# Performance work log

Hardware: AMD Instinct MI355X
Metric: run time of the kernel (lower is better)

## Reference

```python
import jax, jax.numpy as jnp
import numpy as np

NUM_CENTROID = 64
HIDDEN = 768
MAX_SEQ = 128
D = MAX_SEQ * HIDDEN  # 98304 flattened feature dim
NUM_ITERS = 10        # fixed Lloyd iterations (original loops to tol; fixed for jit)


def _cdist(x, c):
    x2 = jnp.sum(x * x, axis=-1, keepdims=True)          # [N,1]
    c2 = jnp.sum(c * c, axis=-1)                          # [K]
    d2 = x2 + c2[None, :] - 2.0 * (x @ c.T)               # [N,K]
    return jnp.sqrt(jnp.maximum(d2, 0.0))


def setup_inputs() -> dict:
    key = jax.random.key(0)
    k1, k2 = jax.random.split(key)
    x = jax.random.normal(k1, (1024, MAX_SEQ, HIDDEN), dtype=jnp.float32)
    # centroid table initialized as Normal(mean=0.07, std=0.39) per the module
    centroid = 0.07 + 0.39 * jax.random.normal(k2, (NUM_CENTROID, D), dtype=jnp.float32)
    return {"x": x, "centroid": centroid}


def reference(x, centroid):
    X = x.reshape(-1, D)                                  # [N, D]
    N = X.shape[0]
    # 'resuming' branch: snap each centroid to its nearest sample
    dis0 = _cdist(X, centroid)                            # [N, K]
    choice_points = jnp.argmin(dis0, axis=0)              # [K]
    state = X[choice_points]                              # [K, D]
    ones = jnp.ones((N,), dtype=X.dtype)

    def step(state, _):
        dis = _cdist(X, state)                            # [N, K]
        choice = jnp.argmin(dis, axis=1)                  # [N]
        sums = jax.ops.segment_sum(X, choice, num_segments=NUM_CENTROID)   # [K, D]
        counts = jax.ops.segment_sum(ones, choice, num_segments=NUM_CENTROID)  # [K]
        nonempty = counts[:, None] > 0
        new_state = jnp.where(nonempty, sums / jnp.maximum(counts[:, None], 1.0), state)
        return new_state, choice

    state, choices = jax.lax.scan(step, state, None, length=NUM_ITERS)
    # returns (new centroids, final cluster assignments) like the module
    return state, choices[-1]
```

## Files before the change

### kernel.cpp

```cpp
#include <hip/hip_runtime.h>
#include <cstddef>
#include <cstdint>


#define N_PTS  1024
#define K_C    64
#define D_DIM  98304
#define ITERS  10
#define SPLITD 64
#define BM     64
#define DC     64
#define LDSP   72
#define NCHK   96
#define CCHK   12
#define NGRP   16
#define SHPG   12
#define SHW    512
#define NCHT   192
#define NPAIR  36
#define GT     128
#define GDC    32

typedef __attribute__((ext_vector_type(8))) short bf16x8;
typedef __attribute__((ext_vector_type(8))) unsigned short ushort8;
typedef __attribute__((ext_vector_type(4))) float f32x4;

__device__ __forceinline__ unsigned short f2bf(float x) {
    unsigned u = __float_as_uint(x);
    u = (u + 0x7FFFu + ((u >> 16) & 1u)) >> 16;
    return (unsigned short)u;
}
__device__ __forceinline__ float bf2f(unsigned short b) {
    return __uint_as_float((unsigned)b << 16);
}
__device__ __forceinline__ void cvt2(float x, unsigned short& h, unsigned short& l) {
    h = f2bf(x);
    l = f2bf(x - bf2f(h));
}

__device__ __forceinline__ void gload_lds16(const unsigned short* g, char* l) {
    __builtin_amdgcn_global_load_lds(
        (const __attribute__((address_space(1))) unsigned int*)g,
        (__attribute__((address_space(3))) unsigned int*)l, 16, 0, 0);
}

__device__ __forceinline__ float block_sum256(float s) {
    #pragma unroll
    for (int o = 32; o; o >>= 1) s += __shfl_down(s, o);
    __shared__ float red[4];
    int lane = threadIdx.x & 63, w = threadIdx.x >> 6;
    if (lane == 0) red[w] = s;
    __syncthreads();
    return red[0] + red[1] + red[2] + red[3];
}

__global__ __launch_bounds__(256) void convert_kernel(const float* __restrict__ A,
                                                      unsigned short* __restrict__ Ph,
                                                      unsigned short* __restrict__ Pl,
                                                      float* __restrict__ sq_part) {
    const int n = blockIdx.x, j = blockIdx.y;
    const size_t base = (size_t)n * D_DIM + (size_t)j * 8192;
    const int t = threadIdx.x;
    float ss = 0.f;
    #pragma unroll
    for (int i = 0; i < 4; ++i) {
        size_t e = base + (size_t)i * 2048 + t * 8;
        float4 a = *reinterpret_cast<const float4*>(A + e);
        float4 b = *reinterpret_cast<const float4*>(A + e + 4);
        ss += a.x*a.x + a.y*a.y + a.z*a.z + a.w*a.w;
        ss += b.x*b.x + b.y*b.y + b.z*b.z + b.w*b.w;
        ushort4 h0, l0, h1, l1;
        cvt2(a.x, h0.x, l0.x); cvt2(a.y, h0.y, l0.y);
        cvt2(a.z, h0.z, l0.z); cvt2(a.w, h0.w, l0.w);
        cvt2(b.x, h1.x, l1.x); cvt2(b.y, h1.y, l1.y);
        cvt2(b.z, h1.z, l1.z); cvt2(b.w, h1.w, l1.w);
        *reinterpret_cast<ushort4*>(Ph + e)     = h0;
        *reinterpret_cast<ushort4*>(Ph + e + 4) = h1;
        *reinterpret_cast<ushort4*>(Pl + e)     = l0;
        *reinterpret_cast<ushort4*>(Pl + e + 4) = l1;
    }
    ss = block_sum256(ss);
    if (t == 0) sq_part[n * CCHK + j] = ss;
}

__global__ __launch_bounds__(256) void reduce_sq_kernel(const float* __restrict__ sq_part,
                                                        float* __restrict__ out, int rows) {
    int n = blockIdx.x * 256 + threadIdx.x;
    if (n >= rows) return;
    float s = 0.f;
    #pragma unroll
    for (int j = 0; j < CCHK; ++j) s += sq_part[n * CCHK + j];
    out[n] = s;
}

__global__ __launch_bounds__(256) void mfma_dot_kernel(const unsigned short* __restrict__ Xh,
                                                       const unsigned short* __restrict__ Xl,
                                                       const unsigned short* __restrict__ Sh,
                                                       const unsigned short* __restrict__ Sl,
                                                       float* __restrict__ partial) {
    __shared__ alignas(16) short Bh[K_C][LDSP];
    __shared__ alignas(16) short Bl[K_C][LDSP];

    const int seg = blockIdx.x, nblk = blockIdx.y;
    const int t = threadIdx.x;
    const int wid = t >> 6, lane = t & 63;
    const int d_begin = seg * (D_DIM / SPLITD);
    const int NCH = (D_DIM / SPLITD) / DC;

    const int arow = nblk * BM + wid * 16 + (lane & 15);
    const int ko = (lane >> 4) * 8;
    const unsigned short* xh = Xh + (size_t)arow * D_DIM;
    const unsigned short* xl = Xl + (size_t)arow * D_DIM;

    const int sr = t >> 2, sc = (t & 3) * 16;
    const unsigned short* shp = Sh + (size_t)sr * D_DIM;
    const unsigned short* slp = Sl + (size_t)sr * D_DIM;

    ushort8 s0, s1, s2, s3;
    bf16x8 aEh0, aEh1, aEl0, aEl1;
    bf16x8 aOh0, aOh1, aOl0, aOl1;

    auto loadB = [&](int d0) {
        s0 = *reinterpret_cast<const ushort8*>(shp + d0 + sc);
        s1 = *reinterpret_cast<const ushort8*>(shp + d0 + sc + 8);
        s2 = *reinterpret_cast<const ushort8*>(slp + d0 + sc);
        s3 = *reinterpret_cast<const ushort8*>(slp + d0 + sc + 8);
    };
    auto storeB = [&]() {
        *reinterpret_cast<ushort8*>(&Bh[sr][sc])     = s0;
        *reinterpret_cast<ushort8*>(&Bh[sr][sc + 8]) = s1;
        *reinterpret_cast<ushort8*>(&Bl[sr][sc])     = s2;
        *reinterpret_cast<ushort8*>(&Bl[sr][sc + 8]) = s3;
    };

    f32x4 acc[4];
    #pragma unroll
    for (int i = 0; i < 4; ++i) acc[i] = f32x4{0.f, 0.f, 0.f, 0.f};

    #define LOADA(bh0, bh1, bl0, bl1, d0)                                        \
        bh0 = *reinterpret_cast<const bf16x8*>(xh + (d0) + ko);                  \
        bh1 = *reinterpret_cast<const bf16x8*>(xh + (d0) + 32 + ko);             \
        bl0 = *reinterpret_cast<const bf16x8*>(xl + (d0) + ko);                  \
        bl1 = *reinterpret_cast<const bf16x8*>(xl + (d0) + 32 + ko);

    #define MFMAS(ah0, ah1, al0, al1)                                            \
        _Pragma("unroll")                                                        \
        for (int nb = 0; nb < 4; ++nb) {                                         \
            const int br = nb * 16 + (lane & 15);                                \
            bf16x8 bh = *reinterpret_cast<const bf16x8*>(&Bh[br][ko]);           \
            bf16x8 bl = *reinterpret_cast<const bf16x8*>(&Bl[br][ko]);           \
            acc[nb] = __builtin_amdgcn_mfma_f32_16x16x32_bf16(ah0, bh, acc[nb], 0, 0, 0); \
            acc[nb] = __builtin_amdgcn_mfma_f32_16x16x32_bf16(ah0, bl, acc[nb], 0, 0, 0); \
            acc[nb] = __builtin_amdgcn_mfma_f32_16x16x32_bf16(al0, bh, acc[nb], 0, 0, 0); \
        }                                                                        \
        _Pragma("unroll")                                                        \
        for (int nb = 0; nb < 4; ++nb) {                                         \
            const int br = nb * 16 + (lane & 15);                                \
            bf16x8 bh = *reinterpret_cast<const bf16x8*>(&Bh[br][32 + ko]);      \
            bf16x8 bl = *reinterpret_cast<const bf16x8*>(&Bl[br][32 + ko]);      \
            acc[nb] = __builtin_amdgcn_mfma_f32_16x16x32_bf16(ah1, bh, acc[nb], 0, 0, 0); \
            acc[nb] = __builtin_amdgcn_mfma_f32_16x16x32_bf16(ah1, bl, acc[nb], 0, 0, 0); \
            acc[nb] = __builtin_amdgcn_mfma_f32_16x16x32_bf16(al1, bh, acc[nb], 0, 0, 0); \
        }

    loadB(d_begin);
    LOADA(aEh0, aEh1, aEl0, aEl1, d_begin);
    for (int c = 0; c < NCH; c += 2) {
        __syncthreads();
        storeB();
        __syncthreads();
        {
            int dn = d_begin + (c + 1) * DC;
            loadB(dn);
            LOADA(aOh0, aOh1, aOl0, aOl1, dn);
        }
        MFMAS(aEh0, aEh1, aEl0, aEl1);
        __syncthreads();
        storeB();
        __syncthreads();
        if (c + 2 < NCH) {
            int dn = d_begin + (c + 2) * DC;
            loadB(dn);
            LOADA(aEh0, aEh1, aEl0, aEl1, dn);
        }
        MFMAS(aOh0, aOh1, aOl0, aOl1);
    }
    #undef LOADA
    #undef MFMAS

    #pragma unroll
    for (int nb = 0; nb < 4; ++nb)
        #pragma unroll
        for (int r = 0; r < 4; ++r) {
            int row = wid * 16 + (lane >> 4) * 4 + r;
            int col = nb * 16 + (lane & 15);
            int n = nblk * BM + row;
            partial[((size_t)seg * N_PTS + n) * K_C + col] = acc[nb][r];
        }
}

__global__ __launch_bounds__(256) void reduce_dot_kernel(const float* __restrict__ partial,
                                                         float* __restrict__ dot) {
    int i = blockIdx.x * 256 + threadIdx.x;
    float s = 0.f;
    #pragma unroll 8
    for (int p = 0; p < SPLITD; ++p) s += partial[(size_t)p * N_PTS * K_C + i];
    dot[i] = s;
}

__global__ __launch_bounds__(256) void argmin_n_kernel(const float* __restrict__ dot,
                                                       const float* __restrict__ x2,
                                                       int* __restrict__ choice_pts) {
    int k = blockIdx.x;
    float best = 3.4e38f; int bi = N_PTS;
    for (int n = threadIdx.x; n < N_PTS; n += 256) {
        float v = fmaf(-2.f, dot[n * K_C + k], x2[n]);
        if (v < best || (v == best && n < bi)) { best = v; bi = n; }
    }
    #pragma unroll
    for (int off = 32; off; off >>= 1) {
        float v2 = __shfl_down(best, off);
        int   i2 = __shfl_down(bi, off);
        if (v2 < best || (v2 == best && i2 < bi)) { best = v2; bi = i2; }
    }
    __shared__ float bv[4]; __shared__ int bix[4];
    int lane = threadIdx.x & 63, wid = threadIdx.x >> 6;
    if (lane == 0) { bv[wid] = best; bix[wid] = bi; }
    __syncthreads();
    if (threadIdx.x == 0) {
        for (int w = 1; w < 4; ++w)
            if (bv[w] < best || (bv[w] == best && bix[w] < bi)) { best = bv[w]; bi = bix[w]; }
        choice_pts[k] = bi;
    }
}

__global__ __launch_bounds__(256) void gather_kernel(const float* __restrict__ X,
                                                     const int* __restrict__ choice_pts,
                                                     float* __restrict__ state) {
    int k = blockIdx.x;
    int c = choice_pts[k];
    size_t d = (size_t)blockIdx.y * 1024 + threadIdx.x * 4;
    float4 v = *reinterpret_cast<const float4*>(X + (size_t)c * D_DIM + d);
    *reinterpret_cast<float4*>(state + (size_t)k * D_DIM + d) = v;
}

__global__ __launch_bounds__(256, 2) void gbuild_kernel(const unsigned short* __restrict__ Xh,
                                                        const unsigned short* __restrict__ Xl,
                                                        float* __restrict__ Gpart) {
    __shared__ alignas(16) char L[65536];

    const int id = blockIdx.x;
    const int xr = id & 7, q = id >> 3;
    const int p = q % NPAIR;
    const int g = ((q / NPAIR) << 3) + xr;
    int bi = 0, rem = p, rl = 8;
    while (rem >= rl) { rem -= rl; --rl; ++bi; }
    const int bj = bi + rem;

    const int t = threadIdx.x;
    const int wid = t >> 6, lane = t & 63;
    const int wr = wid >> 1, wc = wid & 1;

    const int isA = (wid < 2) ? 1 : 0;
    const int i0 = (wid & 1) * 8;
    const int tileoff = isA ? 0 : 16384;
    const int rowbase = (isA ? bi : bj) * GT;
    const int lw = (lane & 7) ^ (lane >> 3);
    const unsigned short* plane = (lw & 4) ? Xl : Xh;
    const unsigned short* gbase[8];
    #pragma unroll
    for (int j = 0; j < 8; ++j)
        gbase[j] = plane + (size_t)(rowbase + (i0 + j) * 8 + (lane >> 3)) * D_DIM + (lw & 3) * 8;

    const int sh = (lane >> 4) ^ (lane & 7);
    const int sl = (4 + (lane >> 4)) ^ (lane & 7);
    const int ra0 = (wr * 64 + (lane & 15)) * 128;
    const int rb0 = 16384 + (wc * 64 + (lane & 15)) * 128;

    f32x4 acc[4][4];
    #pragma unroll
    for (int i = 0; i < 4; ++i)
        #pragma unroll
        for (int j = 0; j < 4; ++j) acc[i][j] = f32x4{0.f, 0.f, 0.f, 0.f};

    auto issue = [&](int idx) {
        const int d0 = (g + ((idx >> 4) << 4)) * SHW + (idx & 15) * GDC;
        char* dst = L + ((idx & 1) << 15) + tileoff + i0 * 1024;
        #pragma unroll
        for (int j = 0; j < 8; ++j)
            gload_lds16(gbase[j] + d0, dst + j * 1024);
    };

    issue(0);
    for (int idx = 0; idx < NCHT; ++idx) {
        if (idx + 1 < NCHT) {
            issue(idx + 1);
            asm volatile("s_waitcnt vmcnt(8)" ::: "memory");
        } else {
            asm volatile("s_waitcnt vmcnt(0)" ::: "memory");
        }
        __builtin_amdgcn_s_barrier();
        __builtin_amdgcn_sched_barrier(0);
        const char* base = L + ((idx & 1) << 15);
        bf16x8 ah[4], al[4];
        #pragma unroll
        for (int fi = 0; fi < 4; ++fi) {
            ah[fi] = *reinterpret_cast<const bf16x8*>(base + ra0 + fi * 2048 + sh * 16);
            al[fi] = *reinterpret_cast<const bf16x8*>(base + ra0 + fi * 2048 + sl * 16);
        }
        #pragma unroll
        for (int fj = 0; fj < 4; ++fj) {
            bf16x8 bh = *reinterpret_cast<const bf16x8*>(base + rb0 + fj * 2048 + sh * 16);
            bf16x8 bl = *reinterpret_cast<const bf16x8*>(base + rb0 + fj * 2048 + sl * 16);
            #pragma unroll
            for (int fi = 0; fi < 4; ++fi) {
                acc[fi][fj] = __builtin_amdgcn_mfma_f32_16x16x32_bf16(ah[fi], bh, acc[fi][fj], 0, 0, 0);
                acc[fi][fj] = __builtin_amdgcn_mfma_f32_16x16x32_bf16(ah[fi], bl, acc[fi][fj], 0, 0, 0);
                acc[fi][fj] = __builtin_amdgcn_mfma_f32_16x16x32_bf16(al[fi], bh, acc[fi][fj], 0, 0, 0);
            }
        }
        __builtin_amdgcn_sched_barrier(0);
        __builtin_amdgcn_s_barrier();
    }

    float* gp = Gpart + ((size_t)g * NPAIR + p) * (GT * GT);
    #pragma unroll
    for (int fi = 0; fi < 4; ++fi)
        #pragma unroll
        for (int fj = 0; fj < 4; ++fj)
            #pragma unroll
            for (int r2 = 0; r2 < 4; ++r2) {
                int row = wr * 64 + fi * 16 + (lane >> 4) * 4 + r2;
                int col = wc * 64 + fj * 16 + (lane & 15);
                gp[row * GT + col] = acc[fi][fj][r2];
            }
}

__global__ __launch_bounds__(256) void reduce_g_kernel(const float* __restrict__ Gpart,
                                                       float* __restrict__ G) {
    const int p = blockIdx.x, blk = blockIdx.y;
    int bi = 0, rem = p, rl = 8;
    while (rem >= rl) { rem -= rl; --rl; ++bi; }
    const int bj = bi + rem;
    const int e0 = blk * 1024 + threadIdx.x * 4;
    float sx = 0.f, sy = 0.f, sz = 0.f, sw = 0.f;
    #pragma unroll 8
    for (int g = 0; g < NGRP; ++g) {
        const float4 v = *reinterpret_cast<const float4*>(
            Gpart + ((size_t)g * NPAIR + p) * (GT * GT) + e0);
        sx += v.x; sy += v.y; sz += v.z; sw += v.w;
    }
    const int row = e0 >> 7, col = e0 & 127;
    const int gi = bi * GT + row, gj = bj * GT + col;
    float4 o = {sx, sy, sz, sw};
    *reinterpret_cast<float4*>(&G[(size_t)gi * N_PTS + gj]) = o;
    if (bi != bj) {
        G[(size_t)(gj + 0) * N_PTS + gi] = sx;
        G[(size_t)(gj + 1) * N_PTS + gi] = sy;
        G[(size_t)(gj + 2) * N_PTS + gi] = sz;
        G[(size_t)(gj + 3) * N_PTS + gi] = sw;
    }
}

__global__ __launch_bounds__(256) void dot0_kernel(const float* __restrict__ G,
                                                   const int* __restrict__ cpts,
                                                   const float* __restrict__ x2,
                                                   float* __restrict__ dot,
                                                   float* __restrict__ c2) {
    int g = blockIdx.x * 256 + threadIdx.x;
    int n = g >> 6, k = g & 63;
    dot[g] = G[(size_t)n * N_PTS + cpts[k]];
    if (g < K_C) c2[g] = x2[cpts[g]];
}

__global__ __launch_bounds__(256) void assign_g_kernel(const float* __restrict__ dot,
                                                       const float* __restrict__ c2,
                                                       int* __restrict__ choice_it) {
    int wid = threadIdx.x >> 6, lane = threadIdx.x & 63;
    int n = blockIdx.x * 4 + wid;
    float v = fmaf(-2.f, dot[n * K_C + lane], c2[lane]);
    int bi = lane;
    #pragma unroll
    for (int m = 32; m; m >>= 1) {
        float v2 = __shfl_xor(v, m);
        int   i2 = __shfl_xor(bi, m);
        if (v2 < v || (v2 == v && i2 < bi)) { v = v2; bi = i2; }
    }
    if (lane == 0) choice_it[n] = bi;
}

__global__ __launch_bounds__(1024) void sort2_kernel(const int* __restrict__ choice,
                                                     int* __restrict__ order,
                                                     int* __restrict__ cstart,
                                                     int* __restrict__ tlast,
                                                     int it) {
    __shared__ int ch[N_PTS];
    __shared__ int cnt[K_C];
    __shared__ int cst[K_C + 1];
    int t = threadIdx.x;
    if (t < K_C) cnt[t] = 0;
    __syncthreads();
    int c = choice[t];
    ch[t] = c;
    atomicAdd(&cnt[c], 1);
    __syncthreads();
    if (t == 0) {
        int a = 0;
        for (int k = 0; k < K_C; ++k) { cst[k] = a; a += cnt[k]; }
        cst[K_C] = a;
    }
    __syncthreads();
    if (t <= K_C) cstart[t] = cst[t];
    if (t < K_C && cnt[t] > 0) tlast[t] = it;
    int r = 0;
    for (int m = 0; m < t; ++m) r += (ch[m] == c);
    order[cst[c] + r] = t;
}

__global__ __launch_bounds__(256) void dotup_kernel(const float* __restrict__ G,
                                                    const int* __restrict__ order,
                                                    const int* __restrict__ cstart,
                                                    float* __restrict__ dot) {
    __shared__ int ord[N_PTS];
    __shared__ int cst[K_C + 1];
    int t = threadIdx.x;
    #pragma unroll
    for (int i = 0; i < 4; ++i) ord[t + 256 * i] = order[t + 256 * i];
    if (t <= K_C) cst[t] = cstart[t];
    __syncthreads();
    int wid = t >> 6, lane = t & 63;
    int n = blockIdx.x * 4 + wid;
    int b = cst[lane], e = cst[lane + 1];
    if (b == e) return;
    const float* gr = G + (size_t)n * N_PTS;
    float s = 0.f;
    for (int i = b; i < e; ++i) s += gr[ord[i]];
    dot[n * K_C + lane] = s / (float)(e - b);
}

__global__ __launch_bounds__(64) void c2up_kernel(const float* __restrict__ dot,
                                                  const int* __restrict__ order,
                                                  const int* __restrict__ cstart,
                                                  float* __restrict__ c2) {
    int k = threadIdx.x;
    int b = cstart[k], e = cstart[k + 1];
    if (b == e) return;
    float s = 0.f;
    for (int i = b; i < e; ++i) s += dot[order[i] * K_C + k];
    c2[k] = s / (float)(e - b);
}

__global__ __launch_bounds__(64) void init_tlast_kernel(int* __restrict__ tlast) {
    tlast[threadIdx.x] = -1;
}

__global__ __launch_bounds__(256) void final_state_kernel(const float* __restrict__ X,
                                                          const int* __restrict__ chbuf,
                                                          const int* __restrict__ tlast,
                                                          float* __restrict__ state) {
    const int k = blockIdx.x;
    const int tk = tlast[k];
    if (tk < 0) return;
    __shared__ int chs[N_PTS];
    const int* src = chbuf + tk * N_PTS;
    const int t = threadIdx.x;
    #pragma unroll
    for (int i = 0; i < 4; ++i) chs[t + 256 * i] = src[t + 256 * i];
    __syncthreads();
    const size_t d = (size_t)blockIdx.y * 1024 + t * 4;
    float sx = 0.f, sy = 0.f, sz = 0.f, sw = 0.f;
    int cm = 0;
    for (int n = 0; n < N_PTS; ++n) {
        if (chs[n] == k) {
            ++cm;
            const float4 v = *reinterpret_cast<const float4*>(X + (size_t)n * D_DIM + d);
            sx += v.x; sy += v.y; sz += v.z; sw += v.w;
        }
    }
    float inv = 1.f / (float)cm;
    float4 o = {sx * inv, sy * inv, sz * inv, sw * inv};
    *reinterpret_cast<float4*>(state + (size_t)k * D_DIM + d) = o;
}

__global__ __launch_bounds__(256) void choice_out_kernel(const int* __restrict__ choice,
                                                         float* __restrict__ out) {
    int n = blockIdx.x * 256 + threadIdx.x;
    if (n < N_PTS) out[n] = (float)choice[n];
}

extern "C" void kernel_launch(void* const* d_in, const int* in_sizes, int n_in,
                              void* d_out, int out_size, void* d_ws, size_t ws_size,
                              hipStream_t stream) {
    const float* X  = (const float*)d_in[0];
    const float* C0 = (const float*)d_in[1];
    float* state      = (float*)d_out;
    float* out_choice = state + (size_t)K_C * D_DIM;

    char* w = (char*)d_ws;
    size_t off = 0;
    auto alloc = [&](size_t bytes) { void* p = w + off; off = (off + bytes + 255) & ~(size_t)255; return p; };
    unsigned short* Xh = (unsigned short*)alloc((size_t)N_PTS * D_DIM * 2);
    unsigned short* Xl = (unsigned short*)alloc((size_t)N_PTS * D_DIM * 2);
    unsigned short* Sh = (unsigned short*)alloc((size_t)K_C * D_DIM * 2);
    unsigned short* Sl = (unsigned short*)alloc((size_t)K_C * D_DIM * 2);
    float* partial = (float*)alloc((size_t)SPLITD * N_PTS * K_C * 4);
    float* Gpart   = (float*)alloc((size_t)NGRP * NPAIR * GT * GT * 4);
    float* G       = (float*)alloc((size_t)N_PTS * N_PTS * 4);
    float* dotb    = (float*)alloc((size_t)N_PTS * K_C * 4);
    float* x2p     = (float*)alloc((size_t)N_PTS * CCHK * 4);
    float* x2      = (float*)alloc((size_t)N_PTS * 4);
    float* c0sq    = (float*)alloc((size_t)K_C * CCHK * 4);
    float* dotg    = (float*)alloc((size_t)N_PTS * K_C * 4);
    float* c2      = (float*)alloc(256);
    int* cpts      = (int*)alloc(256);
    int* chbuf     = (int*)alloc((size_t)ITERS * N_PTS * 4);
    int* order     = (int*)alloc((size_t)N_PTS * 4);
    int* cstart    = (int*)alloc(512);
    int* tlast     = (int*)alloc(256);

    dim3 b256(256);

    convert_kernel<<<dim3(N_PTS, CCHK), b256, 0, stream>>>(X, Xh, Xl, x2p);
    reduce_sq_kernel<<<dim3(4), b256, 0, stream>>>(x2p, x2, N_PTS);

    gbuild_kernel<<<dim3(8 * NPAIR * (NGRP / 8)), b256, 0, stream>>>(Xh, Xl, Gpart);
    reduce_g_kernel<<<dim3(NPAIR, 16), b256, 0, stream>>>(Gpart, G);

    convert_kernel<<<dim3(K_C, CCHK), b256, 0, stream>>>(C0, Sh, Sl, c0sq);
    mfma_dot_kernel<<<dim3(SPLITD, N_PTS / BM), b256, 0, stream>>>(Xh, Xl, Sh, Sl, partial);
    reduce_dot_kernel<<<dim3(N_PTS * K_C / 256), b256, 0, stream>>>(partial, dotb);
    argmin_n_kernel<<<K_C, b256, 0, stream>>>(dotb, x2, cpts);
    gather_kernel<<<dim3(K_C, NCHK), b256, 0, stream>>>(X, cpts, state);
    init_tlast_kernel<<<1, dim3(64), 0, stream>>>(tlast);
    dot0_kernel<<<dim3(N_PTS * K_C / 256), b256, 0, stream>>>(G, cpts, x2, dotg, c2);

    for (int it = 0; it < ITERS; ++it) {
        assign_g_kernel<<<dim3(N_PTS / 4), b256, 0, stream>>>(dotg, c2, chbuf + it * N_PTS);
        sort2_kernel<<<1, dim3(1024), 0, stream>>>(chbuf + it * N_PTS, order, cstart, tlast, it);
        if (it < ITERS - 1) {
            dotup_kernel<<<dim3(N_PTS / 4), b256, 0, stream>>>(G, order, cstart, dotg);
            c2up_kernel<<<1, dim3(64), 0, stream>>>(dotg, order, cstart, c2);
        }
    }

    final_state_kernel<<<dim3(K_C, NCHK), b256, 0, stream>>>(X, chbuf, tlast, state);
    choice_out_kernel<<<dim3(N_PTS / 256), b256, 0, stream>>>(chbuf + (ITERS - 1) * N_PTS, out_choice);
}
```

Measured before the change: 1.898 ms.

## Fuse centroid-dot update into assignment and c2 update into sort kernel

The per-iteration dot update (Gram-row averaging over each cluster's members) moves into the assignment kernel, and the centroid squared-norm update moves into the single-block sort kernel. The initial state is expressed as singleton clusters, so the first assignment uses the same path. This cuts the Lloyd loop from four launches per iteration to two and drops the separate init and choice-output kernels. In exchange, the c2 update now runs inside one 1024-thread block that gathers G rows per point, which serialises that work on a single CU.

```diff
diff --git a/kernel.cpp b/kernel.cpp
--- a/kernel.cpp
+++ b/kernel.cpp
@@ -362,23 +362,49 @@
     }
 }
 
-__global__ __launch_bounds__(256) void dot0_kernel(const float* __restrict__ G,
-                                                   const int* __restrict__ cpts,
-                                                   const float* __restrict__ x2,
-                                                   float* __restrict__ dot,
-                                                   float* __restrict__ c2) {
-    int g = blockIdx.x * 256 + threadIdx.x;
-    int n = g >> 6, k = g & 63;
-    dot[g] = G[(size_t)n * N_PTS + cpts[k]];
-    if (g < K_C) c2[g] = x2[cpts[g]];
-}
-
-__global__ __launch_bounds__(256) void assign_g_kernel(const float* __restrict__ dot,
-                                                       const float* __restrict__ c2,
-                                                       int* __restrict__ choice_it) {
-    int wid = threadIdx.x >> 6, lane = threadIdx.x & 63;
+__global__ __launch_bounds__(64) void init_iter_kernel(const int* __restrict__ cpts,
+                                                       const float* __restrict__ x2,
+                                                       int* __restrict__ order,
+                                                       int* __restrict__ cstart,
+                                                       float* __restrict__ c2,
+                                                       int* __restrict__ tlast) {
+    int k = threadIdx.x;
+    order[k] = cpts[k];
+    cstart[k] = k;
+    if (k == 0) cstart[K_C] = K_C;
+    c2[k] = x2[cpts[k]];
+    tlast[k] = -1;
+}
+
+__global__ __launch_bounds__(256) void assign2_kernel(const float* __restrict__ G,
+                                                      const int* __restrict__ order,
+                                                      const int* __restrict__ cstart,
+                                                      const float* __restrict__ c2,
+                                                      float* __restrict__ dotg,
+                                                      int* __restrict__ choice_it) {
+    __shared__ int ord[N_PTS];
+    __shared__ int cst[K_C + 1];
+    __shared__ float c2s[K_C];
+    int t = threadIdx.x;
+    #pragma unroll
+    for (int i = 0; i < 4; ++i) ord[t + 256 * i] = order[t + 256 * i];
+    if (t <= K_C) cst[t] = cstart[t];
+    if (t < K_C) c2s[t] = c2[t];
+    __syncthreads();
+    int wid = t >> 6, lane = t & 63;
     int n = blockIdx.x * 4 + wid;
-    float v = fmaf(-2.f, dot[n * K_C + lane], c2[lane]);
+    int b = cst[lane], e = cst[lane + 1];
+    float d;
+    if (b == e) {
+        d = dotg[n * K_C + lane];
+    } else {
+        const float* gr = G + (size_t)n * N_PTS;
+        float s = 0.f;
+        for (int i = b; i < e; ++i) s += gr[ord[i]];
+        d = s / (float)(e - b);
+        dotg[n * K_C + lane] = d;
+    }
+    float v = fmaf(-2.f, d, c2s[lane]);
     int bi = lane;
     #pragma unroll
     for (int m = 32; m; m >>= 1) {
@@ -389,18 +415,23 @@
     if (lane == 0) choice_it[n] = bi;
 }
 
-__global__ __launch_bounds__(1024) void sort2_kernel(const int* __restrict__ choice,
-                                                     int* __restrict__ order,
-                                                     int* __restrict__ cstart,
-                                                     int* __restrict__ tlast,
-                                                     int it) {
+__global__ __launch_bounds__(1024) void sortc2_kernel(const float* __restrict__ G,
+                                                      const int* __restrict__ choice,
+                                                      int* __restrict__ order,
+                                                      int* __restrict__ cstart,
+                                                      float* __restrict__ c2,
+                                                      int* __restrict__ tlast,
+                                                      int it,
+                                                      float* __restrict__ out_choice) {
     __shared__ int ch[N_PTS];
+    __shared__ int ords[N_PTS];
+    __shared__ float rs[N_PTS];
     __shared__ int cnt[K_C];
     __shared__ int cst[K_C + 1];
-    int t = threadIdx.x;
+    const int t = threadIdx.x;
     if (t < K_C) cnt[t] = 0;
     __syncthreads();
-    int c = choice[t];
+    const int c = choice[t];
     ch[t] = c;
     atomicAdd(&cnt[c], 1);
     __syncthreads();
@@ -414,44 +445,29 @@
     if (t < K_C && cnt[t] > 0) tlast[t] = it;
     int r = 0;
     for (int m = 0; m < t; ++m) r += (ch[m] == c);
-    order[cst[c] + r] = t;
-}
-
-__global__ __launch_bounds__(256) void dotup_kernel(const float* __restrict__ G,
-                                                    const int* __restrict__ order,
-                                                    const int* __restrict__ cstart,
-                                                    float* __restrict__ dot) {
-    __shared__ int ord[N_PTS];
-    __shared__ int cst[K_C + 1];
-    int t = threadIdx.x;
-    #pragma unroll
-    for (int i = 0; i < 4; ++i) ord[t + 256 * i] = order[t + 256 * i];
-    if (t <= K_C) cst[t] = cstart[t];
-    __syncthreads();
-    int wid = t >> 6, lane = t & 63;
-    int n = blockIdx.x * 4 + wid;
-    int b = cst[lane], e = cst[lane + 1];
-    if (b == e) return;
-    const float* gr = G + (size_t)n * N_PTS;
-    float s = 0.f;
-    for (int i = b; i < e; ++i) s += gr[ord[i]];
-    dot[n * K_C + lane] = s / (float)(e - b);
-}
-
-__global__ __launch_bounds__(64) void c2up_kernel(const float* __restrict__ dot,
-                                                  const int* __restrict__ order,
-                                                  const int* __restrict__ cstart,
-                                                  float* __restrict__ c2) {
-    int k = threadIdx.x;
-    int b = cstart[k], e = cstart[k + 1];
-    if (b == e) return;
-    float s = 0.f;
-    for (int i = b; i < e; ++i) s += dot[order[i] * K_C + k];
-    c2[k] = s / (float)(e - b);
-}
-
-__global__ __launch_bounds__(64) void init_tlast_kernel(int* __restrict__ tlast) {
-    tlast[threadIdx.x] = -1;
+    const int pos = cst[c] + r;
+    ords[pos] = t;
+    order[pos] = t;
+    if (it == ITERS - 1) out_choice[t] = (float)c;
+    if (it < ITERS - 1) {
+        __syncthreads();
+        {
+            const int m = ords[t];
+            const int k = ch[m];
+            const int b = cst[k], e = cst[k + 1];
+            const float* gm = G + (size_t)m * N_PTS;
+            float s = 0.f;
+            for (int i = b; i < e; ++i) s += gm[ords[i]];
+            rs[t] = s / (float)(e - b);
+        }
+        __syncthreads();
+        if (t < K_C && cnt[t] > 0) {
+            const int b = cst[t], e = cst[t + 1];
+            float s = 0.f;
+            for (int i = b; i < e; ++i) s += rs[i];
+            c2[t] = s / (float)(e - b);
+        }
+    }
 }
 
 __global__ __launch_bounds__(256) void final_state_kernel(const float* __restrict__ X,
@@ -480,12 +496,6 @@
     float inv = 1.f / (float)cm;
     float4 o = {sx * inv, sy * inv, sz * inv, sw * inv};
     *reinterpret_cast<float4*>(state + (size_t)k * D_DIM + d) = o;
-}
-
-__global__ __launch_bounds__(256) void choice_out_kernel(const int* __restrict__ choice,
-                                                         float* __restrict__ out) {
-    int n = blockIdx.x * 256 + threadIdx.x;
-    if (n < N_PTS) out[n] = (float)choice[n];
 }
 
 extern "C" void kernel_launch(void* const* d_in, const int* in_sizes, int n_in,
@@ -531,18 +541,14 @@
     reduce_dot_kernel<<<dim3(N_PTS * K_C / 256), b256, 0, stream>>>(partial, dotb);
     argmin_n_kernel<<<K_C, b256, 0, stream>>>(dotb, x2, cpts);
     gather_kernel<<<dim3(K_C, NCHK), b256, 0, stream>>>(X, cpts, state);
-    init_tlast_kernel<<<1, dim3(64), 0, stream>>>(tlast);
-    dot0_kernel<<<dim3(N_PTS * K_C / 256), b256, 0, stream>>>(G, cpts, x2, dotg, c2);
+    init_iter_kernel<<<1, dim3(64), 0, stream>>>(cpts, x2, order, cstart, c2, tlast);
 
     for (int it = 0; it < ITERS; ++it) {
-        assign_g_kernel<<<dim3(N_PTS / 4), b256, 0, stream>>>(dotg, c2, chbuf + it * N_PTS);
-        sort2_kernel<<<1, dim3(1024), 0, stream>>>(chbuf + it * N_PTS, order, cstart, tlast, it);
-        if (it < ITERS - 1) {
-            dotup_kernel<<<dim3(N_PTS / 4), b256, 0, stream>>>(G, order, cstart, dotg);
-            c2up_kernel<<<1, dim3(64), 0, stream>>>(dotg, order, cstart, c2);
-        }
+        assign2_kernel<<<dim3(N_PTS / 4), b256, 0, stream>>>(G, order, cstart, c2, dotg,
+                                                             chbuf + it * N_PTS);
+        sortc2_kernel<<<1, dim3(1024), 0, stream>>>(G, chbuf + it * N_PTS, order, cstart,
+                                                    c2, tlast, it, out_choice);
     }
 
     final_state_kernel<<<dim3(K_C, NCHK), b256, 0, stream>>>(X, chbuf, tlast, state);
-    choice_out_kernel<<<dim3(N_PTS / 256), b256, 0, stream>>>(chbuf + (ITERS - 1) * N_PTS, out_choice);
-}
+}
```

Measured after the change: 2.110 ms. +11.2%, slower.

## Rewrite initial distance GEMM with direct-to-LDS async loads and larger tiles

Applied to the files above, without the earlier changes.

Replaces the initial X·C^T split-bf16 MFMA kernel with a version that streams both the X and centroid tiles straight into swizzled, double-buffered shared memory using global-to-LDS loads, paced by vmcnt waits. Each block now covers 128 rows instead of 64, so every centroid tile it stages serves twice as many points, and the previous register-staged copy with four barriers per pair of chunks goes away. The cost is more hand-written synchronisation and a fixed swizzle layout. It also lowers the number of blocks in the grid (64x8 instead of 64x16), which could reduce occupancy on the device.

```diff
diff --git a/kernel.cpp b/kernel.cpp
--- a/kernel.cpp
+++ b/kernel.cpp
@@ -8,13 +8,9 @@
 #define D_DIM  98304
 #define ITERS  10
 #define SPLITD 64
-#define BM     64
-#define DC     64
-#define LDSP   72
 #define NCHK   96
 #define CCHK   12
 #define NGRP   16
-#define SHPG   12
 #define SHW    512
 #define NCHT   192
 #define NPAIR  36
@@ -93,110 +89,93 @@
     out[n] = s;
 }
 
-__global__ __launch_bounds__(256) void mfma_dot_kernel(const unsigned short* __restrict__ Xh,
-                                                       const unsigned short* __restrict__ Xl,
-                                                       const unsigned short* __restrict__ Sh,
-                                                       const unsigned short* __restrict__ Sl,
-                                                       float* __restrict__ partial) {
-    __shared__ alignas(16) short Bh[K_C][LDSP];
-    __shared__ alignas(16) short Bl[K_C][LDSP];
+__global__ __launch_bounds__(256, 2) void mfma_dot2_kernel(const unsigned short* __restrict__ Xh,
+                                                           const unsigned short* __restrict__ Xl,
+                                                           const unsigned short* __restrict__ Sh,
+                                                           const unsigned short* __restrict__ Sl,
+                                                           float* __restrict__ partial) {
+    __shared__ alignas(16) char L[49152];
 
     const int seg = blockIdx.x, nblk = blockIdx.y;
     const int t = threadIdx.x;
     const int wid = t >> 6, lane = t & 63;
     const int d_begin = seg * (D_DIM / SPLITD);
-    const int NCH = (D_DIM / SPLITD) / DC;
-
-    const int arow = nblk * BM + wid * 16 + (lane & 15);
-    const int ko = (lane >> 4) * 8;
-    const unsigned short* xh = Xh + (size_t)arow * D_DIM;
-    const unsigned short* xl = Xl + (size_t)arow * D_DIM;
-
-    const int sr = t >> 2, sc = (t & 3) * 16;
-    const unsigned short* shp = Sh + (size_t)sr * D_DIM;
-    const unsigned short* slp = Sl + (size_t)sr * D_DIM;
-
-    ushort8 s0, s1, s2, s3;
-    bf16x8 aEh0, aEh1, aEl0, aEl1;
-    bf16x8 aOh0, aOh1, aOl0, aOl1;
-
-    auto loadB = [&](int d0) {
-        s0 = *reinterpret_cast<const ushort8*>(shp + d0 + sc);
-        s1 = *reinterpret_cast<const ushort8*>(shp + d0 + sc + 8);
-        s2 = *reinterpret_cast<const ushort8*>(slp + d0 + sc);
-        s3 = *reinterpret_cast<const ushort8*>(slp + d0 + sc + 8);
+    const int NCH = (D_DIM / SPLITD) / GDC;
+
+    const int isA = (wid < 2) ? 1 : 0;
+    const int nj = isA ? 8 : 4;
+    const int i0 = isA ? (wid & 1) * 8 : (wid & 1) * 4;
+    const int tileoff = isA ? 0 : 16384;
+    const int rowbase = isA ? nblk * 128 : 0;
+    const int lw = (lane & 7) ^ (lane >> 3);
+    const unsigned short* plane = isA ? ((lw & 4) ? Xl : Xh)
+                                      : ((lw & 4) ? Sl : Sh);
+    const unsigned short* gbase[8];
+    #pragma unroll
+    for (int j = 0; j < 8; ++j)
+        gbase[j] = plane + (size_t)(rowbase + (i0 + j) * 8 + (lane >> 3)) * D_DIM + (lw & 3) * 8;
+
+    const int sh = (lane >> 4) ^ (lane & 7);
+    const int sl = (4 + (lane >> 4)) ^ (lane & 7);
+    const int ra0 = (wid * 32 + (lane & 15)) * 128;
+    const int rb0 = 16384 + (lane & 15) * 128;
+
+    f32x4 acc[2][4];
+    #pragma unroll
+    for (int i = 0; i < 2; ++i)
+        #pragma unroll
+        for (int j = 0; j < 4; ++j) acc[i][j] = f32x4{0.f, 0.f, 0.f, 0.f};
+
+    auto issue = [&](int idx) {
+        const int d0 = d_begin + idx * GDC;
+        char* dst = L + (idx & 1) * 24576 + tileoff + i0 * 1024;
+        for (int j = 0; j < nj; ++j)
+            gload_lds16(gbase[j] + d0, dst + j * 1024);
     };
-    auto storeB = [&]() {
-        *reinterpret_cast<ushort8*>(&Bh[sr][sc])     = s0;
-        *reinterpret_cast<ushort8*>(&Bh[sr][sc + 8]) = s1;
-        *reinterpret_cast<ushort8*>(&Bl[sr][sc])     = s2;
-        *reinterpret_cast<ushort8*>(&Bl[sr][sc + 8]) = s3;
-    };
-
-    f32x4 acc[4];
-    #pragma unroll
-    for (int i = 0; i < 4; ++i) acc[i] = f32x4{0.f, 0.f, 0.f, 0.f};
-
-    #define LOADA(bh0, bh1, bl0, bl1, d0)                                        \
-        bh0 = *reinterpret_cast<const bf16x8*>(xh + (d0) + ko);                  \
-        bh1 = *reinterpret_cast<const bf16x8*>(xh + (d0) + 32 + ko);             \
-        bl0 = *reinterpret_cast<const bf16x8*>(xl + (d0) + ko);                  \
-        bl1 = *reinterpret_cast<const bf16x8*>(xl + (d0) + 32 + ko);
-
-    #define MFMAS(ah0, ah1, al0, al1)                                            \
-        _Pragma("unroll")                                                        \
-        for (int nb = 0; nb < 4; ++nb) {                                         \
-            const int br = nb * 16 + (lane & 15);                                \
-            bf16x8 bh = *reinterpret_cast<const bf16x8*>(&Bh[br][ko]);           \
-            bf16x8 bl = *reinterpret_cast<const bf16x8*>(&Bl[br][ko]);           \
-            acc[nb] = __builtin_amdgcn_mfma_f32_16x16x32_bf16(ah0, bh, acc[nb], 0, 0, 0); \
-            acc[nb] = __builtin_amdgcn_mfma_f32_16x16x32_bf16(ah0, bl, acc[nb], 0, 0, 0); \
-            acc[nb] = __builtin_amdgcn_mfma_f32_16x16x32_bf16(al0, bh, acc[nb], 0, 0, 0); \
-        }                                                                        \
-        _Pragma("unroll")                                                        \
-        for (int nb = 0; nb < 4; ++nb) {                                         \
-            const int br = nb * 16 + (lane & 15);                                \
-            bf16x8 bh = *reinterpret_cast<const bf16x8*>(&Bh[br][32 + ko]);      \
-            bf16x8 bl = *reinterpret_cast<const bf16x8*>(&Bl[br][32 + ko]);      \
-            acc[nb] = __builtin_amdgcn_mfma_f32_16x16x32_bf16(ah1, bh, acc[nb], 0, 0, 0); \
-            acc[nb] = __builtin_amdgcn_mfma_f32_16x16x32_bf16(ah1, bl, acc[nb], 0, 0, 0); \
-            acc[nb] = __builtin_amdgcn_mfma_f32_16x16x32_bf16(al1, bh, acc[nb], 0, 0, 0); \
-        }
-
-    loadB(d_begin);
-    LOADA(aEh0, aEh1, aEl0, aEl1, d_begin);
-    for (int c = 0; c < NCH; c += 2) {
-        __syncthreads();
-        storeB();
-        __syncthreads();
-        {
-            int dn = d_begin + (c + 1) * DC;
-            loadB(dn);
-            LOADA(aOh0, aOh1, aOl0, aOl1, dn);
-        }
-        MFMAS(aEh0, aEh1, aEl0, aEl1);
-        __syncthreads();
-        storeB();
-        __syncthreads();
-        if (c + 2 < NCH) {
-            int dn = d_begin + (c + 2) * DC;
-            loadB(dn);
-            LOADA(aEh0, aEh1, aEl0, aEl1, dn);
-        }
-        MFMAS(aOh0, aOh1, aOl0, aOl1);
-    }
-    #undef LOADA
-    #undef MFMAS
-
-    #pragma unroll
-    for (int nb = 0; nb < 4; ++nb)
-        #pragma unroll
-        for (int r = 0; r < 4; ++r) {
-            int row = wid * 16 + (lane >> 4) * 4 + r;
-            int col = nb * 16 + (lane & 15);
-            int n = nblk * BM + row;
-            partial[((size_t)seg * N_PTS + n) * K_C + col] = acc[nb][r];
-        }
+
+    issue(0);
+    for (int idx = 0; idx < NCH; ++idx) {
+        if (idx + 1 < NCH) {
+            issue(idx + 1);
+            if (isA) asm volatile("s_waitcnt vmcnt(8)" ::: "memory");
+            else     asm volatile("s_waitcnt vmcnt(4)" ::: "memory");
+        } else {
+            asm volatile("s_waitcnt vmcnt(0)" ::: "memory");
+        }
+        __builtin_amdgcn_s_barrier();
+        __builtin_amdgcn_sched_barrier(0);
+        const char* base = L + (idx & 1) * 24576;
+        bf16x8 ah[2], al[2];
+        #pragma unroll
+        for (int fi = 0; fi < 2; ++fi) {
+            ah[fi] = *reinterpret_cast<const bf16x8*>(base + ra0 + fi * 2048 + sh * 16);
+            al[fi] = *reinterpret_cast<const bf16x8*>(base + ra0 + fi * 2048 + sl * 16);
+        }
+        #pragma unroll
+        for (int fj = 0; fj < 4; ++fj) {
+            bf16x8 bh = *reinterpret_cast<const bf16x8*>(base + rb0 + fj * 2048 + sh * 16);
+            bf16x8 bl = *reinterpret_cast<const bf16x8*>(base + rb0 + fj * 2048 + sl * 16);
+            #pragma unroll
+            for (int fi = 0; fi < 2; ++fi) {
+                acc[fi][fj] = __builtin_amdgcn_mfma_f32_16x16x32_bf16(ah[fi], bh, acc[fi][fj], 0, 0, 0);
+                acc[fi][fj] = __builtin_amdgcn_mfma_f32_16x16x32_bf16(ah[fi], bl, acc[fi][fj], 0, 0, 0);
+                acc[fi][fj] = __builtin_amdgcn_mfma_f32_16x16x32_bf16(al[fi], bh, acc[fi][fj], 0, 0, 0);
+            }
+        }
+        __builtin_amdgcn_sched_barrier(0);
+        __builtin_amdgcn_s_barrier();
+    }
+
+    #pragma unroll
+    for (int fi = 0; fi < 2; ++fi)
+        #pragma unroll
+        for (int fj = 0; fj < 4; ++fj)
+            #pragma unroll
+            for (int r = 0; r < 4; ++r) {
+                int n = nblk * 128 + wid * 32 + fi * 16 + (lane >> 4) * 4 + r;
+                int col = fj * 16 + (lane & 15);
+                partial[((size_t)seg * N_PTS + n) * K_C + col] = acc[fi][fj][r];
+            }
 }
 
 __global__ __launch_bounds__(256) void reduce_dot_kernel(const float* __restrict__ partial,
@@ -527,7 +506,7 @@
     reduce_g_kernel<<<dim3(NPAIR, 16), b256, 0, stream>>>(Gpart, G);
 
     convert_kernel<<<dim3(K_C, CCHK), b256, 0, stream>>>(C0, Sh, Sl, c0sq);
-    mfma_dot_kernel<<<dim3(SPLITD, N_PTS / BM), b256, 0, stream>>>(Xh, Xl, Sh, Sl, partial);
+    mfma_dot2_kernel<<<dim3(SPLITD, 8), b256, 0, stream>>>(Xh, Xl, Sh, Sl, partial);
     reduce_dot_kernel<<<dim3(N_PTS * K_C / 256), b256, 0, stream>>>(partial, dotb);
     argmin_n_kernel<<<K_C, b256, 0, stream>>>(dotb, x2, cpts);
     gather_kernel<<<dim3(K_C, NCHK), b256, 0, stream>>>(X, cpts, state);
```

After: 1.903 ms. Within noise of the previous version (+0.3%).
